# Optimization experiments

Hardware: AMD Instinct MI355X
Metric: run time of the kernel (lower is better)

Reference implementation:

```python
import jax, jax.numpy as jnp
import numpy as np

EPS = 1e-6
NUM_HEADS = 16

def layer_norm(x, w, b):
    mu = jnp.mean(x, axis=-1, keepdims=True)
    var = jnp.mean(jnp.square(x - mu), axis=-1, keepdims=True)
    return (x - mu) * jax.lax.rsqrt(var + EPS) * w + b

def setup_inputs() -> dict:
    key = jax.random.key(0)
    ks = jax.random.split(key, 8)
    B, N, C = 32, 577, 1024
    H = 4 * C
    s = lambda d: 1.0 / np.sqrt(d)
    return {
        "x": jax.random.normal(ks[0], (B, N, C), jnp.float32),
        "ln1_w": jnp.ones((C,), jnp.float32),
        "ln1_b": jnp.zeros((C,), jnp.float32),
        "qkv_w": jax.random.normal(ks[1], (3 * C, C), jnp.float32) * s(C),
        "qkv_b": jnp.zeros((3 * C,), jnp.float32),
        "proj_w": jax.random.normal(ks[2], (C, C), jnp.float32) * s(C),
        "proj_b": jnp.zeros((C,), jnp.float32),
        "ln2_w": jnp.ones((C,), jnp.float32),
        "ln2_b": jnp.zeros((C,), jnp.float32),
        "fc1_w": jax.random.normal(ks[3], (H, C), jnp.float32) * s(C),
        "fc1_b": jnp.zeros((H,), jnp.float32),
        "fc2_w": jax.random.normal(ks[4], (C, H), jnp.float32) * s(H),
        "fc2_b": jnp.zeros((C,), jnp.float32),
    }

def reference(x, ln1_w, ln1_b, qkv_w, qkv_b, proj_w, proj_b,
              ln2_w, ln2_b, fc1_w, fc1_b, fc2_w, fc2_b):
    B, N, C = x.shape
    Hh = NUM_HEADS
    Dh = C // Hh
    scale = Dh ** -0.5

    # --- attention branch ---
    h = layer_norm(x, ln1_w, ln1_b)
    qkv = h @ qkv_w.T + qkv_b                      # [B,N,3C]
    qkv = qkv.reshape(B, N, 3, Hh, Dh).transpose(2, 0, 3, 1, 4)  # [3,B,H,N,Dh]
    q, k, v = qkv[0] * scale, qkv[1], qkv[2]
    attn = jnp.einsum("bhqd,bhkd->bhqk", q, k)     # [B,H,N,N]
    attn = jax.nn.softmax(attn, axis=-1)
    o = jnp.einsum("bhqk,bhkd->bhqd", attn, v)     # [B,H,N,Dh]
    o = o.transpose(0, 2, 1, 3).reshape(B, N, C)
    x = x + (o @ proj_w.T + proj_b)

    # --- MLP branch ---
    h = layer_norm(x, ln2_w, ln2_b)
    h = jax.nn.gelu(h @ fc1_w.T + fc1_b, approximate=False)
    x = x + (h @ fc2_w.T + fc2_b)
    return x
```

## Files before the change

### kernel.cpp

```cpp
#include <hip/hip_runtime.h>
#include <math.h>

#define BATCH  32
#define NTOK   577
#define CDIM   1024
#define C3DIM  3072
#define H4DIM  4096
#define NHEAD  16
#define MROWS  (BATCH * NTOK)
#define NPADV  584

typedef __bf16 bf16x8 __attribute__((ext_vector_type(8)));
typedef float  f32x4  __attribute__((ext_vector_type(4)));
typedef unsigned short u16x8 __attribute__((ext_vector_type(8)));

__device__ __forceinline__ float bf2f(unsigned short u) {
    union { unsigned int i; float f; } v; v.i = ((unsigned int)u) << 16; return v.f;
}
__device__ __forceinline__ unsigned short f2bf(float f) {
    union { float f; unsigned int i; } v; v.f = f;
    unsigned int r = v.i + 0x7FFFu + ((v.i >> 16) & 1u);
    return (unsigned short)(r >> 16);
}
__device__ __forceinline__ bf16x8 ld_bf8(const unsigned short* p) {
    return __builtin_bit_cast(bf16x8, *(const u16x8*)p);
}

typedef const __attribute__((address_space(1))) unsigned int* gptr_t;
typedef __attribute__((address_space(3))) unsigned int* lptr_t;
__device__ __forceinline__ void gl2lds(const void* g, const void* l) {
    __builtin_amdgcn_global_load_lds(
        (gptr_t)(unsigned long long)g,
        (lptr_t)(unsigned int)(unsigned long long)l,
        16, 0, 0);
}

#define QSCALE 0.18033688011112042f

__global__ __launch_bounds__(256) void conv_kernel(const float* __restrict__ src,
                                                   unsigned short* __restrict__ dst, int n) {
    int i = (blockIdx.x * 256 + threadIdx.x) * 4;
    if (i < n) {
        float4 v = *(const float4*)(src + i);
        dst[i]     = f2bf(v.x);
        dst[i + 1] = f2bf(v.y);
        dst[i + 2] = f2bf(v.z);
        dst[i + 3] = f2bf(v.w);
    }
}

template<bool F32IN>
__global__ __launch_bounds__(256) void ln_kernel(
    const void* __restrict__ X,
    const float* __restrict__ w,
    const float* __restrict__ b,
    unsigned short* __restrict__ out)
{
    const int row = blockIdx.x;
    const int t = threadIdx.x;
    float vals[4]; float s = 0.f, ss = 0.f;
#pragma unroll
    for (int i = 0; i < 4; i++) {
        int c = t + i * 256;
        float v;
        if (F32IN) v = ((const float*)X)[(size_t)row * CDIM + c];
        else       v = bf2f(((const unsigned short*)X)[(size_t)row * CDIM + c]);
        vals[i] = v; s += v; ss += v * v;
    }
#pragma unroll
    for (int off = 32; off > 0; off >>= 1) { s += __shfl_xor(s, off); ss += __shfl_xor(ss, off); }
    __shared__ float red[8];
    if ((t & 63) == 0) { red[t >> 6] = s; red[4 + (t >> 6)] = ss; }
    __syncthreads();
    s  = red[0] + red[1] + red[2] + red[3];
    ss = red[4] + red[5] + red[6] + red[7];
    float mu  = s * (1.f / CDIM);
    float var = ss * (1.f / CDIM) - mu * mu;
    float rs  = rsqrtf(var + 1e-6f);
#pragma unroll
    for (int i = 0; i < 4; i++) {
        int c = t + i * 256;
        float o = (vals[i] - mu) * rs * w[c] + b[c];
        out[(size_t)row * CDIM + c] = f2bf(o);
    }
}

template<int OP>
__global__ __launch_bounds__(256) void gemm_bt(
    const unsigned short* __restrict__ A,
    const unsigned short* __restrict__ W, int Wstride,
    const unsigned short* __restrict__ bias,
    const void* __restrict__ Res,
    void* __restrict__ Out,
    void* __restrict__ Out2,
    void* __restrict__ Out3,
    int K, int Nout)
{
    __shared__ __align__(16) unsigned short Alds[128 * 32];
    __shared__ __align__(16) unsigned short Blds[128 * 32];
    const int tid  = threadIdx.x;
    const int lane = tid & 63, wave = tid >> 6;
    const int q = lane >> 4, l16 = lane & 15;
    const int wm = (wave & 1) << 6, wn = (wave >> 1) << 6;
    const int tileM = blockIdx.y << 7, tileN = blockIdx.x << 7;

    f32x4 acc[4][4];
#pragma unroll
    for (int i = 0; i < 4; i++)
#pragma unroll
        for (int j = 0; j < 4; j++) acc[i][j] = (f32x4){0.f, 0.f, 0.f, 0.f};

    const int srow = tid >> 2;
    const int soff = (tid & 3) << 3;
    int arow1 = tileM + srow;       if (arow1 > MROWS - 1) arow1 = MROWS - 1;
    int arow2 = tileM + srow + 64;  if (arow2 > MROWS - 1) arow2 = MROWS - 1;
    const unsigned short* Aptr  = A + (size_t)arow1 * K + soff;
    const unsigned short* Aptr2 = A + (size_t)arow2 * K + soff;
    const unsigned short* Wp    = W + (size_t)(tileN + srow) * Wstride + soff;
    const unsigned short* Wp2   = Wp + (size_t)64 * Wstride;

    for (int k0 = 0; k0 < K; k0 += 32) {
        __syncthreads();
        gl2lds(Aptr  + k0, &Alds[wave * 512]);
        gl2lds(Aptr2 + k0, &Alds[2048 + wave * 512]);
        gl2lds(Wp    + k0, &Blds[wave * 512]);
        gl2lds(Wp2   + k0, &Blds[2048 + wave * 512]);
        __syncthreads();
        bf16x8 af[4], bfr[4];
#pragma unroll
        for (int mi = 0; mi < 4; mi++) af[mi]  = ld_bf8(&Alds[(wm + mi * 16 + l16) * 32 + q * 8]);
#pragma unroll
        for (int ni = 0; ni < 4; ni++) bfr[ni] = ld_bf8(&Blds[(wn + ni * 16 + l16) * 32 + q * 8]);
#pragma unroll
        for (int mi = 0; mi < 4; mi++)
#pragma unroll
            for (int ni = 0; ni < 4; ni++)
                acc[mi][ni] = __builtin_amdgcn_mfma_f32_16x16x32_bf16(af[mi], bfr[ni], acc[mi][ni], 0, 0, 0);
    }

#pragma unroll
    for (int mi = 0; mi < 4; mi++) {
#pragma unroll
        for (int r = 0; r < 4; r++) {
            int row = tileM + wm + mi * 16 + q * 4 + r;
            if (row >= MROWS) continue;
            unsigned int bb = 0, nn = 0;
            if constexpr (OP == 0) {
                bb = ((unsigned int)row * 58154u) >> 25;
                nn = (unsigned int)row - bb * 577u;
            }
#pragma unroll
            for (int ni = 0; ni < 4; ni++) {
                int col = tileN + wn + ni * 16 + l16;
                size_t oidx = (size_t)row * Nout + col;
                float v = acc[mi][ni][r];
                if constexpr (OP != 4) v += bf2f(bias[col]);
                if constexpr (OP == 0) {
                    int s = col >> 10, h = (col >> 6) & 15, d = col & 63;
                    size_t bh = (size_t)(bb * 16 + h);
                    if (s == 0)      ((unsigned short*)Out )[(bh * NTOK + nn) * 64 + d] = f2bf(v * QSCALE);
                    else if (s == 1) ((unsigned short*)Out2)[(bh * NTOK + nn) * 64 + d] = f2bf(v);
                    else             ((unsigned short*)Out3)[(bh * 64 + d) * NPADV + nn] = f2bf(v);
                } else if constexpr (OP == 1) {
                    v += ((const float*)Res)[oidx];
                    ((unsigned short*)Out)[oidx] = f2bf(v);
                } else if constexpr (OP == 2) {
                    v = 0.5f * v * (1.0f + erff(v * 0.70710678118654752f));
                    ((unsigned short*)Out)[oidx] = f2bf(v);
                } else if constexpr (OP == 3) {
                    v += bf2f(((const unsigned short*)Res)[oidx]);
                    ((float*)Out)[oidx] = v;
                } else {
                    ((float*)Out)[oidx] += v;
                }
            }
        }
    }
}

__global__ __launch_bounds__(256) void attn_kernel(
    const unsigned short* __restrict__ Qb,
    const unsigned short* __restrict__ Kb,
    const unsigned short* __restrict__ Vt,
    unsigned short* __restrict__ o)
{
    const int flat = blockIdx.x;
    const int x8 = flat & 7;
    const int g = flat >> 3;
    const int qt = g % 10;
    const int bh = (g / 10) * 8 + x8;
    const int q0 = qt * 64;
    const int tid = threadIdx.x;
    const int wv = tid >> 6, lane = tid & 63;
    const int qd = lane >> 4, l16 = lane & 15;

    __shared__ __align__(16) unsigned short Ps[4][16 * 72];

    const unsigned short* Qh = Qb + (size_t)bh * NTOK * 64;
    const unsigned short* Kh = Kb + (size_t)bh * NTOK * 64;
    const unsigned short* Vh = Vt + (size_t)bh * 64 * NPADV;

    int qrow = q0 + wv * 16 + l16;
    int qr = qrow < NTOK ? qrow : NTOK - 1;
    bf16x8 qf0 = ld_bf8(Qh + (size_t)qr * 64 + qd * 8);
    bf16x8 qf1 = ld_bf8(Qh + (size_t)qr * 64 + 32 + qd * 8);

    float lsum[4];
    f32x4 Oacc[4];
#pragma unroll
    for (int r = 0; r < 4; r++) lsum[r] = 0.f;
#pragma unroll
    for (int ni = 0; ni < 4; ni++) Oacc[ni] = (f32x4){0.f, 0.f, 0.f, 0.f};

    for (int kt = 0; kt < 10; kt++) {
        const int k0 = kt * 64;
        const bool tail = (kt == 9);
        f32x4 sacc[4];
#pragma unroll
        for (int ni = 0; ni < 4; ni++) sacc[ni] = (f32x4){0.f, 0.f, 0.f, 0.f};
#pragma unroll
        for (int ni = 0; ni < 4; ni++) {
            int krow = k0 + ni * 16 + l16;
            if (krow > NTOK - 1) krow = NTOK - 1;
            const unsigned short* kp = Kh + (size_t)krow * 64 + qd * 8;
            bf16x8 b0 = ld_bf8(kp);
            bf16x8 b1 = ld_bf8(kp + 32);
            sacc[ni] = __builtin_amdgcn_mfma_f32_16x16x32_bf16(qf0, b0, sacc[ni], 0, 0, 0);
            sacc[ni] = __builtin_amdgcn_mfma_f32_16x16x32_bf16(qf1, b1, sacc[ni], 0, 0, 0);
        }

#pragma unroll
        for (int r = 0; r < 4; r++) {
#pragma unroll
            for (int ni = 0; ni < 4; ni++) {
                float pv = exp2f(sacc[ni][r]);
                if (tail && (k0 + ni * 16 + l16 >= NTOK)) pv = 0.f;
                lsum[r] += pv;
                Ps[wv][(qd * 4 + r) * 72 + ni * 16 + l16] = f2bf(pv);
            }
        }

#pragma unroll
        for (int kk = 0; kk < 2; kk++) {
            bf16x8 a = ld_bf8(&Ps[wv][l16 * 72 + kk * 32 + qd * 8]);
            int kchunk = k0 + kk * 32 + qd * 8;
            if (kchunk > NTOK - 1) kchunk = NTOK - 1;
#pragma unroll
            for (int ni = 0; ni < 4; ni++) {
                bf16x8 bb = ld_bf8(Vh + (size_t)(ni * 16 + l16) * NPADV + kchunk);
                Oacc[ni] = __builtin_amdgcn_mfma_f32_16x16x32_bf16(a, bb, Oacc[ni], 0, 0, 0);
            }
        }
    }

#pragma unroll
    for (int r = 0; r < 4; r++)
#pragma unroll
        for (int off = 8; off > 0; off >>= 1) lsum[r] += __shfl_xor(lsum[r], off);

    const int b = bh >> 4, h = bh & 15;
#pragma unroll
    for (int r = 0; r < 4; r++) {
        int gq = q0 + wv * 16 + qd * 4 + r;
        if (gq >= NTOK) continue;
        float inv = 1.0f / lsum[r];
#pragma unroll
        for (int ni = 0; ni < 4; ni++) {
            int d = ni * 16 + l16;
            o[((size_t)b * NTOK + gq) * CDIM + (size_t)h * 64 + d] = f2bf(Oacc[ni][r] * inv);
        }
    }
}

extern "C" void kernel_launch(void* const* d_in, const int* in_sizes, int n_in,
                              void* d_out, int out_size, void* d_ws, size_t ws_size,
                              hipStream_t stream) {
    (void)in_sizes; (void)n_in; (void)out_size;
    const float* x      = (const float*)d_in[0];
    const float* ln1_w  = (const float*)d_in[1];
    const float* ln1_b  = (const float*)d_in[2];
    const float* qkv_w  = (const float*)d_in[3];
    const float* qkv_b  = (const float*)d_in[4];
    const float* proj_w = (const float*)d_in[5];
    const float* proj_b = (const float*)d_in[6];
    const float* ln2_w  = (const float*)d_in[7];
    const float* ln2_b  = (const float*)d_in[8];
    const float* fc1_w  = (const float*)d_in[9];
    const float* fc1_b  = (const float*)d_in[10];
    const float* fc2_w  = (const float*)d_in[11];
    const float* fc2_b  = (const float*)d_in[12];

    char* ws = (char*)d_ws;
    size_t off = 0;
    auto alloc = [&](size_t els) { void* p = ws + off; off += els * 2; return (unsigned short*)p; };
    unsigned short* qkvw_b  = alloc(3145728);
    unsigned short* projw_b = alloc(1048576);
    unsigned short* fc1w_b  = alloc(4194304);
    unsigned short* fc2w_b  = alloc(4194304);
    unsigned short* qkvb_b  = alloc(3072);
    unsigned short* projb_b = alloc(1024);
    unsigned short* fc1b_b  = alloc(4096);
    unsigned short* fc2b_b  = alloc(1024);
    off = (off + 255) & ~(size_t)255;
    unsigned short* R1 = (unsigned short*)(ws + off); off += (size_t)MROWS * 1024 * 2;
    unsigned short* R2 = (unsigned short*)(ws + off); off += (size_t)512 * 64 * NPADV * 2;
    unsigned short* R3 = (unsigned short*)(ws + off);
    size_t rem = ws_size > off ? ws_size - off : 0;
    const int CH = rem >= (size_t)MROWS * H4DIM * 2 ? H4DIM
                 : (rem >= (size_t)MROWS * 1024 * 2 ? 1024
                 : (rem >= (size_t)MROWS * 512 * 2 ? 512 : 256));

    unsigned short* Qb   = (unsigned short*)d_out;
    unsigned short* h1   = Qb + (size_t)MROWS * 1024;
    unsigned short* obuf = h1;
    unsigned short* Kb = R1;
    unsigned short* Vt = R2;
    unsigned short* x1 = R1;
    unsigned short* h2 = R2;

    conv_kernel<<<3145728 / 1024, 256, 0, stream>>>(qkv_w,  qkvw_b,  3145728);
    conv_kernel<<<1048576 / 1024, 256, 0, stream>>>(proj_w, projw_b, 1048576);
    conv_kernel<<<4194304 / 1024, 256, 0, stream>>>(fc1_w,  fc1w_b,  4194304);
    conv_kernel<<<4194304 / 1024, 256, 0, stream>>>(fc2_w,  fc2w_b,  4194304);
    conv_kernel<<<3, 256, 0, stream>>>(qkv_b,  qkvb_b,  3072);
    conv_kernel<<<1, 256, 0, stream>>>(proj_b, projb_b, 1024);
    conv_kernel<<<4, 256, 0, stream>>>(fc1_b,  fc1b_b,  4096);
    conv_kernel<<<1, 256, 0, stream>>>(fc2_b,  fc2b_b,  1024);

    const int mt = (MROWS + 127) / 128;

    ln_kernel<true><<<MROWS, 256, 0, stream>>>(x, ln1_w, ln1_b, h1);
    gemm_bt<0><<<dim3(C3DIM / 128, mt), 256, 0, stream>>>(
        h1, qkvw_b, CDIM, qkvb_b, nullptr, Qb, Kb, Vt, CDIM, C3DIM);
    attn_kernel<<<5120, 256, 0, stream>>>(Qb, Kb, Vt, obuf);
    gemm_bt<1><<<dim3(CDIM / 128, mt), 256, 0, stream>>>(
        obuf, projw_b, CDIM, projb_b, x, x1, nullptr, nullptr, CDIM, CDIM);
    ln_kernel<false><<<MROWS, 256, 0, stream>>>(x1, ln2_w, ln2_b, h2);

    if (CH == H4DIM) {
        gemm_bt<2><<<dim3(H4DIM / 128, mt), 256, 0, stream>>>(
            h2, fc1w_b, CDIM, fc1b_b, nullptr, R3, nullptr, nullptr, CDIM, H4DIM);
        gemm_bt<3><<<dim3(CDIM / 128, mt), 256, 0, stream>>>(
            R3, fc2w_b, H4DIM, fc2b_b, x1, d_out, nullptr, nullptr, H4DIM, CDIM);
    } else {
        for (int c0 = 0; c0 < H4DIM; c0 += CH) {
            gemm_bt<2><<<dim3(CH / 128, mt), 256, 0, stream>>>(
                h2, fc1w_b + (size_t)c0 * CDIM, CDIM, fc1b_b + c0, nullptr, R3, nullptr, nullptr, CDIM, CH);
            if (c0 == 0)
                gemm_bt<3><<<dim3(CDIM / 128, mt), 256, 0, stream>>>(
                    R3, fc2w_b, H4DIM, fc2b_b, x1, d_out, nullptr, nullptr, CH, CDIM);
            else
                gemm_bt<4><<<dim3(CDIM / 128, mt), 256, 0, stream>>>(
                    R3, fc2w_b + c0, H4DIM, nullptr, nullptr, d_out, nullptr, nullptr, CH, CDIM);
        }
    }
}
```

Baseline: 1.293 ms.

## Enlarge GEMM tiles to 256x256 with double-buffered LDS pipeline and fast GELU

Replaces the 128x128 single-buffered GEMM with a 256x256-tile, 512-thread kernel that double-buffers 64-wide K slices in LDS, so global-to-LDS loads overlap with MFMA compute and each loaded element is reused across more outputs. Each wave now computes a 128x64 sub-tile. The exact erf GELU is replaced with a sigmoid-style exp2 approximation. The larger tiles use much more LDS (128KB per block) and more registers, and they leave fewer blocks in the grid. The GELU change adds approximation error.

New measurement: 1.263 ms. -2.3%, faster.

```diff
diff --git a/kernel.cpp b/kernel.cpp
--- a/kernel.cpp
+++ b/kernel.cpp
@@ -86,7 +86,7 @@
 }
 
 template<int OP>
-__global__ __launch_bounds__(256) void gemm_bt(
+__global__ __launch_bounds__(512, 2) void gemm256(
     const unsigned short* __restrict__ A,
     const unsigned short* __restrict__ W, int Wstride,
     const unsigned short* __restrict__ bias,
@@ -96,50 +96,72 @@
     void* __restrict__ Out3,
     int K, int Nout)
 {
-    __shared__ __align__(16) unsigned short Alds[128 * 32];
-    __shared__ __align__(16) unsigned short Blds[128 * 32];
+    __shared__ __align__(16) unsigned short Alds[2][256 * 64];
+    __shared__ __align__(16) unsigned short Blds[2][256 * 64];
+
     const int tid  = threadIdx.x;
     const int lane = tid & 63, wave = tid >> 6;
     const int q = lane >> 4, l16 = lane & 15;
-    const int wm = (wave & 1) << 6, wn = (wave >> 1) << 6;
-    const int tileM = blockIdx.y << 7, tileN = blockIdx.x << 7;
-
-    f32x4 acc[4][4];
-#pragma unroll
-    for (int i = 0; i < 4; i++)
+    const int wm = (wave >> 2) << 7;
+    const int wn = (wave & 3) << 6;
+    const int tileM = blockIdx.y << 8, tileN = blockIdx.x << 8;
+
+    f32x4 acc[8][4];
+#pragma unroll
+    for (int i = 0; i < 8; i++)
 #pragma unroll
         for (int j = 0; j < 4; j++) acc[i][j] = (f32x4){0.f, 0.f, 0.f, 0.f};
 
-    const int srow = tid >> 2;
-    const int soff = (tid & 3) << 3;
-    int arow1 = tileM + srow;       if (arow1 > MROWS - 1) arow1 = MROWS - 1;
-    int arow2 = tileM + srow + 64;  if (arow2 > MROWS - 1) arow2 = MROWS - 1;
-    const unsigned short* Aptr  = A + (size_t)arow1 * K + soff;
-    const unsigned short* Aptr2 = A + (size_t)arow2 * K + soff;
-    const unsigned short* Wp    = W + (size_t)(tileN + srow) * Wstride + soff;
-    const unsigned short* Wp2   = Wp + (size_t)64 * Wstride;
-
-    for (int k0 = 0; k0 < K; k0 += 32) {
+    const int srow = tid >> 3;
+    const int scol = (tid & 7) << 3;
+    const unsigned short* pA[4];
+    const unsigned short* pB[4];
+#pragma unroll
+    for (int j = 0; j < 4; j++) {
+        int ra = tileM + j * 64 + srow; if (ra > MROWS - 1) ra = MROWS - 1;
+        pA[j] = A + (size_t)ra * K + scol;
+        pB[j] = W + (size_t)(tileN + j * 64 + srow) * Wstride + scol;
+    }
+
+    auto STAGE = [&](int buf, int k0) {
+#pragma unroll
+        for (int j = 0; j < 4; j++) {
+            gl2lds(pA[j] + k0, &Alds[buf][j * 4096 + wave * 512]);
+            gl2lds(pB[j] + k0, &Blds[buf][j * 4096 + wave * 512]);
+        }
+    };
+
+    auto COMPUTE = [&](int buf) {
+#pragma unroll
+        for (int ks = 0; ks < 2; ks++) {
+            bf16x8 af[8], bfr[4];
+#pragma unroll
+            for (int mi = 0; mi < 8; mi++)
+                af[mi] = ld_bf8(&Alds[buf][(wm + mi * 16 + l16) * 64 + ks * 32 + q * 8]);
+#pragma unroll
+            for (int ni = 0; ni < 4; ni++)
+                bfr[ni] = ld_bf8(&Blds[buf][(wn + ni * 16 + l16) * 64 + ks * 32 + q * 8]);
+#pragma unroll
+            for (int mi = 0; mi < 8; mi++)
+#pragma unroll
+                for (int ni = 0; ni < 4; ni++)
+                    acc[mi][ni] = __builtin_amdgcn_mfma_f32_16x16x32_bf16(af[mi], bfr[ni], acc[mi][ni], 0, 0, 0);
+        }
+    };
+
+    const int NT = K >> 6;
+    STAGE(0, 0);
+    __syncthreads();
+    int cur = 0;
+    for (int t = 0; t < NT; ++t) {
+        if (t + 1 < NT) STAGE(cur ^ 1, (t + 1) << 6);
+        COMPUTE(cur);
         __syncthreads();
-        gl2lds(Aptr  + k0, &Alds[wave * 512]);
-        gl2lds(Aptr2 + k0, &Alds[2048 + wave * 512]);
-        gl2lds(Wp    + k0, &Blds[wave * 512]);
-        gl2lds(Wp2   + k0, &Blds[2048 + wave * 512]);
-        __syncthreads();
-        bf16x8 af[4], bfr[4];
-#pragma unroll
-        for (int mi = 0; mi < 4; mi++) af[mi]  = ld_bf8(&Alds[(wm + mi * 16 + l16) * 32 + q * 8]);
-#pragma unroll
-        for (int ni = 0; ni < 4; ni++) bfr[ni] = ld_bf8(&Blds[(wn + ni * 16 + l16) * 32 + q * 8]);
-#pragma unroll
-        for (int mi = 0; mi < 4; mi++)
-#pragma unroll
-            for (int ni = 0; ni < 4; ni++)
-                acc[mi][ni] = __builtin_amdgcn_mfma_f32_16x16x32_bf16(af[mi], bfr[ni], acc[mi][ni], 0, 0, 0);
-    }
-
-#pragma unroll
-    for (int mi = 0; mi < 4; mi++) {
+        cur ^= 1;
+    }
+
+#pragma unroll
+    for (int mi = 0; mi < 8; mi++) {
 #pragma unroll
         for (int r = 0; r < 4; r++) {
             int row = tileM + wm + mi * 16 + q * 4 + r;
@@ -165,7 +187,8 @@
                     v += ((const float*)Res)[oidx];
                     ((unsigned short*)Out)[oidx] = f2bf(v);
                 } else if constexpr (OP == 2) {
-                    v = 0.5f * v * (1.0f + erff(v * 0.70710678118654752f));
+                    float z = exp2f(v * fmaf(v * v, 0.1029432f, 2.3022082f));
+                    v = v - v * __builtin_amdgcn_rcpf(1.0f + z);
                     ((unsigned short*)Out)[oidx] = f2bf(v);
                 } else if constexpr (OP == 3) {
                     v += bf2f(((const unsigned short*)Res)[oidx]);
@@ -327,30 +350,30 @@
     conv_kernel<<<4, 256, 0, stream>>>(fc1_b,  fc1b_b,  4096);
     conv_kernel<<<1, 256, 0, stream>>>(fc2_b,  fc2b_b,  1024);
 
-    const int mt = (MROWS + 127) / 128;
+    const int mt = (MROWS + 255) / 256;
 
     ln_kernel<true><<<MROWS, 256, 0, stream>>>(x, ln1_w, ln1_b, h1);
-    gemm_bt<0><<<dim3(C3DIM / 128, mt), 256, 0, stream>>>(
+    gemm256<0><<<dim3(C3DIM / 256, mt), 512, 0, stream>>>(
         h1, qkvw_b, CDIM, qkvb_b, nullptr, Qb, Kb, Vt, CDIM, C3DIM);
     attn_kernel<<<5120, 256, 0, stream>>>(Qb, Kb, Vt, obuf);
-    gemm_bt<1><<<dim3(CDIM / 128, mt), 256, 0, stream>>>(
+    gemm256<1><<<dim3(CDIM / 256, mt), 512, 0, stream>>>(
         obuf, projw_b, CDIM, projb_b, x, x1, nullptr, nullptr, CDIM, CDIM);
     ln_kernel<false><<<MROWS, 256, 0, stream>>>(x1, ln2_w, ln2_b, h2);
 
     if (CH == H4DIM) {
-        gemm_bt<2><<<dim3(H4DIM / 128, mt), 256, 0, stream>>>(
+        gemm256<2><<<dim3(H4DIM / 256, mt), 512, 0, stream>>>(
             h2, fc1w_b, CDIM, fc1b_b, nullptr, R3, nullptr, nullptr, CDIM, H4DIM);
-        gemm_bt<3><<<dim3(CDIM / 128, mt), 256, 0, stream>>>(
+        gemm256<3><<<dim3(CDIM / 256, mt), 512, 0, stream>>>(
             R3, fc2w_b, H4DIM, fc2b_b, x1, d_out, nullptr, nullptr, H4DIM, CDIM);
     } else {
         for (int c0 = 0; c0 < H4DIM; c0 += CH) {
-            gemm_bt<2><<<dim3(CH / 128, mt), 256, 0, stream>>>(
+            gemm256<2><<<dim3(CH / 256, mt), 512, 0, stream>>>(
                 h2, fc1w_b + (size_t)c0 * CDIM, CDIM, fc1b_b + c0, nullptr, R3, nullptr, nullptr, CDIM, CH);
             if (c0 == 0)
-                gemm_bt<3><<<dim3(CDIM / 128, mt), 256, 0, stream>>>(
+                gemm256<3><<<dim3(CDIM / 256, mt), 512, 0, stream>>>(
                     R3, fc2w_b, H4DIM, fc2b_b, x1, d_out, nullptr, nullptr, CH, CDIM);
             else
-                gemm_bt<4><<<dim3(CDIM / 128, mt), 256, 0, stream>>>(
+                gemm256<4><<<dim3(CDIM / 256, mt), 512, 0, stream>>>(
                     R3, fc2w_b + c0, H4DIM, nullptr, nullptr, d_out, nullptr, nullptr, CH, CDIM);
         }
     }
```
